# Kernel tuning notes

Hardware: AMD Instinct MI355X
Metric: run time of the kernel (lower is better)

## Reference

```python
import jax, jax.numpy as jnp
import numpy as np

OBS, ACT, HID, MIX, TOPK = 64, 16, 256, 16, 4
EPS = 1e-5

def _ln(x, g, b):
    m = jnp.mean(x, axis=-1, keepdims=True)
    v = jnp.mean(jnp.square(x - m), axis=-1, keepdims=True)
    return (x - m) * jax.lax.rsqrt(v + EPS) * g + b

def setup_inputs() -> dict:
    key = jax.random.key(0)
    ks = jax.random.split(key, 12)
    B = 16384
    D = OBS + ACT            # 80
    F = HID * MIX            # 4096
    s = lambda fan_in: 1.0 / np.sqrt(fan_in)
    return {
        "x": jax.random.normal(ks[0], (B, OBS), jnp.float32),
        "a": jax.random.normal(ks[1], (B, ACT), jnp.float32),
        "W1": jax.random.uniform(ks[2], (F, D), jnp.float32, -s(D), s(D)),
        "b1": jnp.zeros((F,), jnp.float32),
        "W2": jax.random.uniform(ks[3], (F, F), jnp.float32, -s(F), s(F)),
        "b2": jnp.zeros((F,), jnp.float32),
        "W3": jax.random.uniform(ks[4], (1, HID), jnp.float32, -s(HID), s(HID)),
        "b3": jnp.zeros((1,), jnp.float32),
        "g1": jnp.ones((F,), jnp.float32),
        "be1": jnp.zeros((F,), jnp.float32),
        "g2": jnp.ones((F,), jnp.float32),
        "be2": jnp.zeros((F,), jnp.float32),
        "Wg": jax.random.uniform(ks[5], (MIX, D), jnp.float32, -s(D), s(D)),
        "bg": jnp.zeros((MIX,), jnp.float32),
    }

def reference(x, a, W1, b1, W2, b2, W3, b3, g1, be1, g2, be2, Wg, bg):
    B = x.shape[0]
    xa = jnp.concatenate([x, a], axis=1)                      # [B, D]
    gate_scores = jax.nn.softmax(xa @ Wg.T + bg, axis=-1)     # [B, MIX]
    topk_vals, topk_idx = jax.lax.top_k(gate_scores, TOPK)    # [B, K]
    # renormalize top-k weights, scatter into dense score tensor
    topk_vals = topk_vals / jnp.sum(topk_vals, axis=-1, keepdims=True)
    scores = jnp.zeros_like(gate_scores).at[
        jnp.arange(B)[:, None], topk_idx].set(topk_vals)      # [B, MIX]
    h = jax.nn.relu(_ln(xa @ W1.T + b1, g1, be1))             # [B, HID*MIX]
    h = jax.nn.relu(_ln(h @ W2.T + b2, g2, be2))              # [B, HID*MIX]
    h = h.reshape(B, HID, MIX)                                # row-major, same as torch
    h = jnp.mean(h * scores[:, None, :], axis=-1)             # [B, HID]
    return h @ W3.T + b3                                      # [B, 1]
```

## Files before the change

### kernel.cpp

```cpp
#include <hip/hip_runtime.h>
#include <stdint.h>

#define OBS 64
#define ACTD 16
#define DIN 80
#define MIX 16
#define FF 4096
#define NB 16384
#define CHUNK 4096
#define KP 96
#define LNEPS 1e-5f

typedef float f32x4 __attribute__((ext_vector_type(4)));
typedef short bf16x8 __attribute__((ext_vector_type(8)));

__device__ __forceinline__ unsigned short f2bf(float f) {
    union { float f; uint32_t u; } v; v.f = f;
    uint32_t u = v.u;
    u += 0x7fff + ((u >> 16) & 1);
    return (unsigned short)(u >> 16);
}
__device__ __forceinline__ float bf2f(unsigned short h) {
    union { uint32_t u; float f; } v; v.u = ((uint32_t)h) << 16;
    return v.f;
}

__global__ __launch_bounds__(256) void k_conv(const float* __restrict__ W,
                                              unsigned short* __restrict__ O, int n4) {
    int i = blockIdx.x * 256 + threadIdx.x;
    if (i >= n4) return;
    float4 v = ((const float4*)W)[i];
    ushort4 o;
    o.x = f2bf(v.x); o.y = f2bf(v.y); o.z = f2bf(v.z); o.w = f2bf(v.w);
    ((ushort4*)O)[i] = o;
}

__global__ __launch_bounds__(256) void k_prep_x(const float* __restrict__ x, const float* __restrict__ a,
                                                unsigned short* __restrict__ xab) {
    int row = blockIdx.x * 256 + threadIdx.x;
    const float4* xp = (const float4*)(x + (size_t)row * OBS);
    unsigned short* o = xab + (size_t)row * KP;
#pragma unroll
    for (int i = 0; i < 16; ++i) {
        float4 v = xp[i];
        ushort4 u; u.x = f2bf(v.x); u.y = f2bf(v.y); u.z = f2bf(v.z); u.w = f2bf(v.w);
        ((ushort4*)o)[i] = u;
    }
    const float4* ap = (const float4*)(a + (size_t)row * ACTD);
#pragma unroll
    for (int i = 0; i < 4; ++i) {
        float4 v = ap[i];
        ushort4 u; u.x = f2bf(v.x); u.y = f2bf(v.y); u.z = f2bf(v.z); u.w = f2bf(v.w);
        ((ushort4*)(o + OBS))[i] = u;
    }
    ushort4 t0; t0.x = 0x3F80; t0.y = 0; t0.z = 0; t0.w = 0;
    ushort4 z;  z.x = 0; z.y = 0; z.z = 0; z.w = 0;
    ((ushort4*)(o + 80))[0] = t0;
    ((ushort4*)(o + 84))[0] = z;
    ((ushort4*)(o + 88))[0] = z;
    ((ushort4*)(o + 92))[0] = z;
}

__global__ __launch_bounds__(256) void k_prep_w1(const float* __restrict__ W1, const float* __restrict__ b1,
                                                 unsigned short* __restrict__ W1b) {
    int f = blockIdx.x * 256 + threadIdx.x;
    const float4* wp = (const float4*)(W1 + (size_t)f * DIN);
    unsigned short* o = W1b + (size_t)f * KP;
#pragma unroll
    for (int i = 0; i < 20; ++i) {
        float4 v = wp[i];
        ushort4 u; u.x = f2bf(v.x); u.y = f2bf(v.y); u.z = f2bf(v.z); u.w = f2bf(v.w);
        ((ushort4*)o)[i] = u;
    }
    ushort4 t0; t0.x = f2bf(b1[f]); t0.y = 0; t0.z = 0; t0.w = 0;
    ushort4 z;  z.x = 0; z.y = 0; z.z = 0; z.w = 0;
    ((ushort4*)(o + 80))[0] = t0;
    ((ushort4*)(o + 84))[0] = z;
    ((ushort4*)(o + 88))[0] = z;
    ((ushort4*)(o + 92))[0] = z;
}

__global__ __launch_bounds__(256) void k_gate(const float* __restrict__ x, const float* __restrict__ a,
                                              const float* __restrict__ Wg, const float* __restrict__ bg,
                                              float* __restrict__ scores) {
    __shared__ float wgs[MIX * DIN];
    __shared__ float bgs[MIX];
    int t = threadIdx.x;
    for (int e = t; e < MIX * DIN; e += 256) wgs[e] = Wg[e];
    if (t < MIX) bgs[t] = bg[t];
    __syncthreads();
    int row = blockIdx.x * 256 + t;
    float xa[DIN];
    const float4* xp = (const float4*)(x + (size_t)row * OBS);
#pragma unroll
    for (int i = 0; i < OBS / 4; ++i) {
        float4 v = xp[i];
        xa[i*4] = v.x; xa[i*4+1] = v.y; xa[i*4+2] = v.z; xa[i*4+3] = v.w;
    }
    const float4* ap = (const float4*)(a + (size_t)row * ACTD);
#pragma unroll
    for (int i = 0; i < ACTD / 4; ++i) {
        float4 v = ap[i];
        xa[OBS+i*4] = v.x; xa[OBS+i*4+1] = v.y; xa[OBS+i*4+2] = v.z; xa[OBS+i*4+3] = v.w;
    }
    double p[MIX];
    double mx = -1e300;
#pragma unroll
    for (int m = 0; m < MIX; ++m) {
        double acc = (double)bgs[m];
#pragma unroll
        for (int k = 0; k < DIN; ++k) acc += (double)xa[k] * (double)wgs[m*DIN + k];
        p[m] = acc;
        if (acc > mx) mx = acc;
    }
#pragma unroll
    for (int m = 0; m < MIX; ++m) p[m] = exp(p[m] - mx);
    unsigned used = 0;
    double s4 = 0.0;
#pragma unroll
    for (int j = 0; j < 4; ++j) {
        int best = 0; double bv = -1.0;
#pragma unroll
        for (int m = 0; m < MIX; ++m)
            if (!((used >> m) & 1) && p[m] > bv) { bv = p[m]; best = m; }
        used |= 1u << best;
        s4 += bv;
    }
    float* so = scores + (size_t)row * MIX;
#pragma unroll
    for (int m = 0; m < MIX; ++m)
        so[m] = ((used >> m) & 1) ? (float)(p[m] / s4) : 0.f;
}

__global__ __launch_bounds__(256) void k_gemm1(const unsigned short* __restrict__ A,
                                               const unsigned short* __restrict__ B,
                                               unsigned short* __restrict__ C,
                                               float* __restrict__ pstats) {
    __shared__ alignas(16) unsigned short As[128 * 32];
    __shared__ alignas(16) unsigned short Bs[128 * 32];
    int t = threadIdx.x;
    int pm = blockIdx.x & 31;
    int pn = blockIdx.x >> 5;
    int lane = t & 63, wid = t >> 6, wm = wid >> 1, wn = wid & 1;

    const unsigned short* Ap = A + (size_t)pm * 128 * KP;
    const unsigned short* Bp = B + (size_t)pn * 128 * KP;

    f32x4 acc[4][4] = {};

    for (int k0 = 0; k0 < KP; k0 += 32) {
#pragma unroll
        for (int i = 0; i < 2; ++i) {
            int u = t + i * 256;
            int row = u >> 2, p = u & 3;
            int ls = p ^ ((row >> 1) & 3);
            __builtin_amdgcn_global_load_lds(
                (const __attribute__((address_space(1))) void*)(Ap + (size_t)row * KP + k0 + ls * 8),
                (__attribute__((address_space(3))) void*)(As + u * 8), 16, 0, 0);
            __builtin_amdgcn_global_load_lds(
                (const __attribute__((address_space(1))) void*)(Bp + (size_t)row * KP + k0 + ls * 8),
                (__attribute__((address_space(3))) void*)(Bs + u * 8), 16, 0, 0);
        }
        __syncthreads();
        bf16x8 af[4], bfr[4];
#pragma unroll
        for (int mf = 0; mf < 4; ++mf) {
            int r = wm * 64 + mf * 16 + (lane & 15);
            int p = (lane >> 4) ^ ((r >> 1) & 3);
            af[mf] = *(const bf16x8*)(As + r * 32 + p * 8);
        }
#pragma unroll
        for (int nf = 0; nf < 4; ++nf) {
            int r = wn * 64 + nf * 16 + (lane & 15);
            int p = (lane >> 4) ^ ((r >> 1) & 3);
            bfr[nf] = *(const bf16x8*)(Bs + r * 32 + p * 8);
        }
#pragma unroll
        for (int mf = 0; mf < 4; ++mf)
#pragma unroll
            for (int nf = 0; nf < 4; ++nf)
                acc[mf][nf] = __builtin_amdgcn_mfma_f32_16x16x32_bf16(af[mf], bfr[nf], acc[mf][nf], 0, 0, 0);
        __syncthreads();
    }

    int rowbase = pm * 128 + wm * 64 + (lane >> 4) * 4;
    int colbase = pn * 128 + wn * 64 + (lane & 15);
#pragma unroll
    for (int mf = 0; mf < 4; ++mf) {
#pragma unroll
        for (int rr = 0; rr < 4; ++rr) {
            float ss = 0.f, qq = 0.f;
#pragma unroll
            for (int nf = 0; nf < 4; ++nf) {
                float v = acc[mf][nf][rr];
                ss += v; qq += v * v;
                C[(size_t)(rowbase + mf * 16 + rr) * FF + colbase + nf * 16] = f2bf(v);
            }
#pragma unroll
            for (int mask = 1; mask <= 8; mask <<= 1) {
                ss += __shfl_xor(ss, mask);
                qq += __shfl_xor(qq, mask);
            }
            if ((lane & 15) == 0) {
                int row = rowbase + mf * 16 + rr;
                int j = pn * 2 + wn;
                pstats[((size_t)row * 64 + j) * 2 + 0] = ss;
                pstats[((size_t)row * 64 + j) * 2 + 1] = qq;
            }
        }
    }
}

__global__ __launch_bounds__(256) void k_ln1(unsigned short* __restrict__ h1,
                                             const float* __restrict__ pstats,
                                             const float* __restrict__ g1, const float* __restrict__ be1) {
    __shared__ float st[8][2];
    int t = threadIdx.x;
    int r0 = blockIdx.x * 8;
    if (t < 8) {
        float s = 0.f, q = 0.f;
        const float* pp = pstats + (size_t)(r0 + t) * 128;
#pragma unroll
        for (int j = 0; j < 64; ++j) { s += pp[j * 2]; q += pp[j * 2 + 1]; }
        float mu = s / (float)FF;
        float var = q / (float)FF - mu * mu;
        st[t][0] = mu;
        st[t][1] = rsqrtf(var + LNEPS);
    }
    __syncthreads();
    int c = t * 16;
    float g[16], b[16];
#pragma unroll
    for (int q = 0; q < 4; ++q) {
        float4 gv = *(const float4*)(g1 + c + q * 4);
        float4 bv = *(const float4*)(be1 + c + q * 4);
        g[q*4] = gv.x; g[q*4+1] = gv.y; g[q*4+2] = gv.z; g[q*4+3] = gv.w;
        b[q*4] = bv.x; b[q*4+1] = bv.y; b[q*4+2] = bv.z; b[q*4+3] = bv.w;
    }
    for (int r = 0; r < 8; ++r) {
        float mu = st[r][0], rs = st[r][1];
        unsigned short* hp = h1 + (size_t)(r0 + r) * FF + c;
        uint4 u0 = *(const uint4*)hp;
        uint4 u1 = *(const uint4*)(hp + 8);
        uint32_t uu[8] = {u0.x, u0.y, u0.z, u0.w, u1.x, u1.y, u1.z, u1.w};
        uint32_t oo[8];
#pragma unroll
        for (int q = 0; q < 8; ++q) {
            float v0 = bf2f((unsigned short)(uu[q] & 0xffff));
            float v1 = bf2f((unsigned short)(uu[q] >> 16));
            float o0 = fmaxf((v0 - mu) * rs * g[q*2]   + b[q*2],   0.f);
            float o1 = fmaxf((v1 - mu) * rs * g[q*2+1] + b[q*2+1], 0.f);
            oo[q] = (uint32_t)f2bf(o0) | ((uint32_t)f2bf(o1) << 16);
        }
        uint4 w0; w0.x = oo[0]; w0.y = oo[1]; w0.z = oo[2]; w0.w = oo[3];
        uint4 w1; w1.x = oo[4]; w1.y = oo[5]; w1.z = oo[6]; w1.w = oo[7];
        *(uint4*)hp = w0;
        *(uint4*)(hp + 8) = w1;
    }
}

__global__ __launch_bounds__(512, 1) void k_gemm2(const unsigned short* __restrict__ A,
                                                  const unsigned short* __restrict__ B,
                                                  unsigned short* __restrict__ C) {
    constexpr int K = FF;
    constexpr int NKT = K / 64;
    __shared__ alignas(16) unsigned short As[2][2][8192];
    __shared__ alignas(16) unsigned short Bs[2][2][8192];

    int t = threadIdx.x;
    int lane = t & 63, wid = t >> 6;
    int wm = wid >> 2, wn = wid & 3;

    int bid = blockIdx.x;
    int xcd = bid & 7, w = bid >> 3;
    int pm = (xcd >> 1) * 4 + (w >> 3);
    int pn = (xcd & 1) * 8 + (w & 7);

    const unsigned short* Ap = A + (size_t)pm * 256 * K;
    const unsigned short* Bp = B + (size_t)pn * 256 * K;

    int l15 = lane & 15, l4 = lane >> 4;
    int slk0 = (l4 ^ (l15 & 7)) * 16;
    int slk1 = ((4 + l4) ^ (l15 & 7)) * 16;
    const char* Abase = (const char*)&As[0][0][0];
    const char* Bbase = (const char*)&Bs[0][0][0];
    const char* afp0 = Abase + wm * 16384 + l15 * 128 + slk0;
    const char* afp1 = Abase + wm * 16384 + l15 * 128 + slk1;
    const char* bfp0 = Bbase + (wn >> 1) * 16384 + (wn & 1) * 8192 + l15 * 128 + slk0;
    const char* bfp1 = Bbase + (wn >> 1) * 16384 + (wn & 1) * 8192 + l15 * 128 + slk1;

    int r0 = t >> 3;
    int swz = ((t & 7) ^ (r0 & 7)) * 8;
    const unsigned short* sA0 = Ap + (size_t)(r0)       * K + swz;
    const unsigned short* sA1 = Ap + (size_t)(64 + r0)  * K + swz;
    const unsigned short* sA2 = Ap + (size_t)(128 + r0) * K + swz;
    const unsigned short* sA3 = Ap + (size_t)(192 + r0) * K + swz;
    const unsigned short* sB0 = Bp + (size_t)(r0)       * K + swz;
    const unsigned short* sB1 = Bp + (size_t)(64 + r0)  * K + swz;
    const unsigned short* sB2 = Bp + (size_t)(128 + r0) * K + swz;
    const unsigned short* sB3 = Bp + (size_t)(192 + r0) * K + swz;
    char* dA = (char*)&As[0][0][0] + t * 16;
    char* dB = (char*)&Bs[0][0][0] + t * 16;

    f32x4 acc[8][4] = {};
    bf16x8 af[4][2], bfr[4][2];

#define STG_A(BUF, HH, p0, p1)                                                              \
    __builtin_amdgcn_global_load_lds((const __attribute__((address_space(1))) void*)(p0),   \
        (__attribute__((address_space(3))) void*)(dA + (BUF)*32768 + (HH)*16384), 16, 0, 0);\
    __builtin_amdgcn_global_load_lds((const __attribute__((address_space(1))) void*)(p1),   \
        (__attribute__((address_space(3))) void*)(dA + (BUF)*32768 + (HH)*16384 + 8192), 16, 0, 0);
#define STG_B(BUF, HH, p0, p1)                                                              \
    __builtin_amdgcn_global_load_lds((const __attribute__((address_space(1))) void*)(p0),   \
        (__attribute__((address_space(3))) void*)(dB + (BUF)*32768 + (HH)*16384), 16, 0, 0);\
    __builtin_amdgcn_global_load_lds((const __attribute__((address_space(1))) void*)(p1),   \
        (__attribute__((address_space(3))) void*)(dB + (BUF)*32768 + (HH)*16384 + 8192), 16, 0, 0);

#define RD_AF(BUF, MH)                                                                      \
    _Pragma("unroll") for (int m = 0; m < 4; ++m) {                                         \
        af[m][0] = *(const bf16x8*)(afp0 + (BUF)*32768 + (MH)*8192 + m*2048);               \
        af[m][1] = *(const bf16x8*)(afp1 + (BUF)*32768 + (MH)*8192 + m*2048);               \
    }
#define RD_BF(BUF)                                                                          \
    _Pragma("unroll") for (int n2 = 0; n2 < 4; ++n2) {                                      \
        bfr[n2][0] = *(const bf16x8*)(bfp0 + (BUF)*32768 + n2*2048);                        \
        bfr[n2][1] = *(const bf16x8*)(bfp1 + (BUF)*32768 + n2*2048);                        \
    }

#define MFMA_Q(MB, NLO)                                                                     \
    __builtin_amdgcn_s_setprio(1);                                                          \
    _Pragma("unroll") for (int kk = 0; kk < 2; ++kk)                                        \
    _Pragma("unroll") for (int m = 0; m < 4; ++m)                                           \
    _Pragma("unroll") for (int n = (NLO); n < (NLO) + 2; ++n)                               \
        acc[(MB)*4 + m][n] = __builtin_amdgcn_mfma_f32_16x16x32_bf16(                       \
            af[m][kk], bfr[n][kk], acc[(MB)*4 + m][n], 0, 0, 0);                            \
    __builtin_amdgcn_s_setprio(0);                                                          \
    __builtin_amdgcn_sched_barrier(0);

#define TILE(BUF, DO_STAGE)                                                                 \
    if (DO_STAGE) { STG_A(1 - (BUF), 0, sA0, sA1) }                                         \
    if (DO_STAGE) asm volatile("s_waitcnt vmcnt(2)" ::: "memory");                          \
    else          asm volatile("s_waitcnt vmcnt(0)" ::: "memory");                          \
    __builtin_amdgcn_s_barrier();                                                           \
    __builtin_amdgcn_sched_barrier(0);                                                      \
    RD_AF(BUF, 0) RD_BF(BUF)                                                                \
    MFMA_Q(0, 0)                                                                            \
    if (DO_STAGE) { STG_A(1 - (BUF), 1, sA2, sA3) }                                         \
    MFMA_Q(0, 2)                                                                            \
    if (DO_STAGE) { STG_B(1 - (BUF), 0, sB0, sB1) }                                         \
    RD_AF(BUF, 1)                                                                           \
    MFMA_Q(1, 0)                                                                            \
    if (DO_STAGE) { STG_B(1 - (BUF), 1, sB2, sB3) }                                         \
    MFMA_Q(1, 2)                                                                            \
    asm volatile("" ::: "memory");                                                          \
    __builtin_amdgcn_s_barrier();                                                           \
    asm volatile("" ::: "memory");                                                          \
    if (DO_STAGE) { sA0 += 64; sA1 += 64; sA2 += 64; sA3 += 64;                             \
                    sB0 += 64; sB1 += 64; sB2 += 64; sB3 += 64; }

    STG_A(0, 0, sA0, sA1) STG_A(0, 1, sA2, sA3)
    STG_B(0, 0, sB0, sB1) STG_B(0, 1, sB2, sB3)
    sA0 += 64; sA1 += 64; sA2 += 64; sA3 += 64;
    sB0 += 64; sB1 += 64; sB2 += 64; sB3 += 64;
    asm volatile("" ::: "memory");

    for (int i = 0; i < NKT / 2 - 1; ++i) {
        TILE(0, true)
        TILE(1, true)
    }
    TILE(0, true)
    TILE(1, false)

#undef STG_A
#undef STG_B
#undef RD_AF
#undef RD_BF
#undef MFMA_Q
#undef TILE

    int row0 = pm * 256 + wm * 128 + (lane >> 4) * 4;
    int col0 = pn * 256 + wn * 64 + (lane & 15);
#pragma unroll
    for (int gm = 0; gm < 8; ++gm)
#pragma unroll
        for (int gn = 0; gn < 4; ++gn)
#pragma unroll
            for (int rr = 0; rr < 4; ++rr)
                C[(size_t)(row0 + gm * 16 + rr) * FF + col0 + gn * 16] = f2bf(acc[gm][gn][rr]);
}

__global__ __launch_bounds__(256) void k_epi(const unsigned short* __restrict__ y2,
                                             const float* __restrict__ scores,
                                             const float* __restrict__ b2,
                                             const float* __restrict__ g2, const float* __restrict__ be2,
                                             const float* __restrict__ W3, const float* __restrict__ b3,
                                             float* __restrict__ out) {
    int row = blockIdx.x, t = threadIdx.x;
    int lane = t & 63, wid = t >> 6;
    __shared__ float sS[MIX];
    __shared__ float rA[4], rB[4];
    __shared__ float stats[2];
    const unsigned short* yp = y2 + (size_t)row * FF + t * 16;
    uint4 u0 = *(const uint4*)yp;
    uint4 u1 = *(const uint4*)(yp + 8);
    float v[16];
    v[0]  = bf2f((unsigned short)(u0.x & 0xffff)); v[1]  = bf2f((unsigned short)(u0.x >> 16));
    v[2]  = bf2f((unsigned short)(u0.y & 0xffff)); v[3]  = bf2f((unsigned short)(u0.y >> 16));
    v[4]  = bf2f((unsigned short)(u0.z & 0xffff)); v[5]  = bf2f((unsigned short)(u0.z >> 16));
    v[6]  = bf2f((unsigned short)(u0.w & 0xffff)); v[7]  = bf2f((unsigned short)(u0.w >> 16));
    v[8]  = bf2f((unsigned short)(u1.x & 0xffff)); v[9]  = bf2f((unsigned short)(u1.x >> 16));
    v[10] = bf2f((unsigned short)(u1.y & 0xffff)); v[11] = bf2f((unsigned short)(u1.y >> 16));
    v[12] = bf2f((unsigned short)(u1.z & 0xffff)); v[13] = bf2f((unsigned short)(u1.z >> 16));
    v[14] = bf2f((unsigned short)(u1.w & 0xffff)); v[15] = bf2f((unsigned short)(u1.w >> 16));
    const float* b2p = b2 + t * 16;
#pragma unroll
    for (int blk = 0; blk < 4; ++blk) {
        float4 q = *(const float4*)(b2p + blk * 4);
        v[blk*4+0] += q.x; v[blk*4+1] += q.y; v[blk*4+2] += q.z; v[blk*4+3] += q.w;
    }
    if (t < MIX) sS[t] = scores[(size_t)row * MIX + t];
    float s = 0.f, sq = 0.f;
#pragma unroll
    for (int j = 0; j < 16; ++j) { s += v[j]; sq += v[j] * v[j]; }
#pragma unroll
    for (int off = 32; off >= 1; off >>= 1) {
        s  += __shfl_down(s, off);
        sq += __shfl_down(sq, off);
    }
    if (lane == 0) { rA[wid] = s; rB[wid] = sq; }
    __syncthreads();
    if (t == 0) {
        float S = rA[0] + rA[1] + rA[2] + rA[3];
        float Q = rB[0] + rB[1] + rB[2] + rB[3];
        float mu = S / (float)FF;
        float var = Q / (float)FF - mu * mu;
        stats[0] = mu;
        stats[1] = rsqrtf(var + LNEPS);
    }
    __syncthreads();
    float mu = stats[0], rs = stats[1];
    const float* gp = g2 + t * 16;
    const float* bp = be2 + t * 16;
    float accum = 0.f;
#pragma unroll
    for (int blk = 0; blk < 4; ++blk) {
        float4 gg = *(const float4*)(gp + blk * 4);
        float4 bb = *(const float4*)(bp + blk * 4);
        float ga[4] = {gg.x, gg.y, gg.z, gg.w};
        float ba[4] = {bb.x, bb.y, bb.z, bb.w};
#pragma unroll
        for (int jj = 0; jj < 4; ++jj) {
            int m = blk * 4 + jj;
            float o = (v[m] - mu) * rs * ga[jj] + ba[jj];
            o = fmaxf(o, 0.f);
            accum += o * sS[m];
        }
    }
    float part = accum * W3[t] * 0.0625f;
#pragma unroll
    for (int off = 32; off >= 1; off >>= 1) part += __shfl_down(part, off);
    if (lane == 0) rA[wid] = part;
    __syncthreads();
    if (t == 0) out[row] = rA[0] + rA[1] + rA[2] + rA[3] + b3[0];
}

extern "C" void kernel_launch(void* const* d_in, const int* in_sizes, int n_in,
                              void* d_out, int out_size, void* d_ws, size_t ws_size,
                              hipStream_t stream) {
    const float* x   = (const float*)d_in[0];
    const float* a   = (const float*)d_in[1];
    const float* W1  = (const float*)d_in[2];
    const float* b1  = (const float*)d_in[3];
    const float* W2  = (const float*)d_in[4];
    const float* b2  = (const float*)d_in[5];
    const float* W3  = (const float*)d_in[6];
    const float* b3  = (const float*)d_in[7];
    const float* g1  = (const float*)d_in[8];
    const float* be1 = (const float*)d_in[9];
    const float* g2  = (const float*)d_in[10];
    const float* be2 = (const float*)d_in[11];
    const float* Wg  = (const float*)d_in[12];
    const float* bg  = (const float*)d_in[13];
    float* out = (float*)d_out;

    char* ws = (char*)d_ws;
    unsigned short* W2b    = (unsigned short*)ws;
    float*          scores = (float*)(ws + 33554432ull);
    unsigned short* h1c    = (unsigned short*)(ws + 34603008ull);
    unsigned short* y2c    = (unsigned short*)(ws + 68157440ull);
    unsigned short* xabc   = (unsigned short*)(ws + 68157440ull);
    unsigned short* W1b    = (unsigned short*)(ws + 68157440ull + 786432ull);
    float*          pstats = (float*)(ws + 68157440ull + 1572864ull);

    k_conv<<<(FF * FF / 4 + 255) / 256, 256, 0, stream>>>(W2, W2b, FF * FF / 4);
    k_gate<<<NB / 256, 256, 0, stream>>>(x, a, Wg, bg, scores);

    for (int c = 0; c < NB / CHUNK; ++c) {
        const float* xc = x + (size_t)c * CHUNK * OBS;
        const float* ac = a + (size_t)c * CHUNK * ACTD;
        const float* sc = scores + (size_t)c * CHUNK * MIX;
        float* oc = out + (size_t)c * CHUNK;
        k_prep_x<<<CHUNK / 256, 256, 0, stream>>>(xc, ac, xabc);
        k_prep_w1<<<FF / 256, 256, 0, stream>>>(W1, b1, W1b);
        k_gemm1<<<(CHUNK / 128) * (FF / 128), 256, 0, stream>>>(xabc, W1b, h1c, pstats);
        k_ln1<<<CHUNK / 8, 256, 0, stream>>>(h1c, pstats, g1, be1);
        k_gemm2<<<(CHUNK / 256) * (FF / 256), 512, 0, stream>>>(h1c, W2b, y2c);
        k_epi<<<CHUNK, 256, 0, stream>>>(y2c, sc, b2, g2, be2, W3, b3, oc);
    }
}
```

Before: 742.6 us.

## Restructure GEMM main loop into finer-grained LDS staging with per-quarter barriers

```diff
diff --git a/kernel.cpp b/kernel.cpp
--- a/kernel.cpp
+++ b/kernel.cpp
@@ -321,62 +321,79 @@
         af[m][0] = *(const bf16x8*)(afp0 + (BUF)*32768 + (MH)*8192 + m*2048);               \
         af[m][1] = *(const bf16x8*)(afp1 + (BUF)*32768 + (MH)*8192 + m*2048);               \
     }
-#define RD_BF(BUF)                                                                          \
-    _Pragma("unroll") for (int n2 = 0; n2 < 4; ++n2) {                                      \
-        bfr[n2][0] = *(const bf16x8*)(bfp0 + (BUF)*32768 + n2*2048);                        \
-        bfr[n2][1] = *(const bf16x8*)(bfp1 + (BUF)*32768 + n2*2048);                        \
-    }
-
-#define MFMA_Q(MB, NLO)                                                                     \
+#define RD_BF2(BUF, NP)                                                                     \
+    _Pragma("unroll") for (int n2 = 0; n2 < 2; ++n2) {                                      \
+        bfr[(NP)*2 + n2][0] = *(const bf16x8*)(bfp0 + (BUF)*32768 + ((NP)*2 + n2)*2048);    \
+        bfr[(NP)*2 + n2][1] = *(const bf16x8*)(bfp1 + (BUF)*32768 + ((NP)*2 + n2)*2048);    \
+    }
+
+#define MFMA_Q(MB, NP)                                                                      \
+    __builtin_amdgcn_s_barrier();                                                           \
+    asm volatile("s_waitcnt lgkmcnt(0)" ::: "memory");                                      \
+    __builtin_amdgcn_sched_barrier(0);                                                      \
     __builtin_amdgcn_s_setprio(1);                                                          \
     _Pragma("unroll") for (int kk = 0; kk < 2; ++kk)                                        \
     _Pragma("unroll") for (int m = 0; m < 4; ++m)                                           \
-    _Pragma("unroll") for (int n = (NLO); n < (NLO) + 2; ++n)                               \
-        acc[(MB)*4 + m][n] = __builtin_amdgcn_mfma_f32_16x16x32_bf16(                       \
-            af[m][kk], bfr[n][kk], acc[(MB)*4 + m][n], 0, 0, 0);                            \
+    _Pragma("unroll") for (int n = 0; n < 2; ++n)                                           \
+        acc[(MB)*4 + m][(NP)*2 + n] = __builtin_amdgcn_mfma_f32_16x16x32_bf16(              \
+            af[m][kk], bfr[(NP)*2 + n][kk], acc[(MB)*4 + m][(NP)*2 + n], 0, 0, 0);          \
     __builtin_amdgcn_s_setprio(0);                                                          \
     __builtin_amdgcn_sched_barrier(0);
-
-#define TILE(BUF, DO_STAGE)                                                                 \
-    if (DO_STAGE) { STG_A(1 - (BUF), 0, sA0, sA1) }                                         \
-    if (DO_STAGE) asm volatile("s_waitcnt vmcnt(2)" ::: "memory");                          \
-    else          asm volatile("s_waitcnt vmcnt(0)" ::: "memory");                          \
-    __builtin_amdgcn_s_barrier();                                                           \
-    __builtin_amdgcn_sched_barrier(0);                                                      \
-    RD_AF(BUF, 0) RD_BF(BUF)                                                                \
-    MFMA_Q(0, 0)                                                                            \
-    if (DO_STAGE) { STG_A(1 - (BUF), 1, sA2, sA3) }                                         \
-    MFMA_Q(0, 2)                                                                            \
-    if (DO_STAGE) { STG_B(1 - (BUF), 0, sB0, sB1) }                                         \
-    RD_AF(BUF, 1)                                                                           \
-    MFMA_Q(1, 0)                                                                            \
-    if (DO_STAGE) { STG_B(1 - (BUF), 1, sB2, sB3) }                                         \
-    MFMA_Q(1, 2)                                                                            \
-    asm volatile("" ::: "memory");                                                          \
-    __builtin_amdgcn_s_barrier();                                                           \
-    asm volatile("" ::: "memory");                                                          \
-    if (DO_STAGE) { sA0 += 64; sA1 += 64; sA2 += 64; sA3 += 64;                             \
-                    sB0 += 64; sB1 += 64; sB2 += 64; sB3 += 64; }
 
     STG_A(0, 0, sA0, sA1) STG_A(0, 1, sA2, sA3)
     STG_B(0, 0, sB0, sB1) STG_B(0, 1, sB2, sB3)
     sA0 += 64; sA1 += 64; sA2 += 64; sA3 += 64;
     sB0 += 64; sB1 += 64; sB2 += 64; sB3 += 64;
-    asm volatile("" ::: "memory");
-
-    for (int i = 0; i < NKT / 2 - 1; ++i) {
-        TILE(0, true)
-        TILE(1, true)
-    }
-    TILE(0, true)
-    TILE(1, false)
-
+    STG_B(1, 0, sB0, sB1) STG_B(1, 1, sB2, sB3)
+    sB0 += 64; sB1 += 64; sB2 += 64; sB3 += 64;
+    asm volatile("s_waitcnt vmcnt(4)" ::: "memory");
+    __builtin_amdgcn_s_barrier();
+
+    for (int i = 0; i < NKT / 2; ++i) {
+        RD_AF(0, 0) RD_BF2(0, 0)
+        STG_A(1, 0, sA0, sA1)
+        MFMA_Q(0, 0)
+        __builtin_amdgcn_s_barrier();
+        RD_BF2(0, 1)
+        STG_A(1, 1, sA2, sA3)
+        MFMA_Q(0, 1)
+        __builtin_amdgcn_s_barrier();
+        sA0 += 64; sA1 += 64; sA2 += 64; sA3 += 64;
+        RD_AF(0, 1)
+        STG_B(0, 0, sB0, sB1)
+        MFMA_Q(1, 0)
+        __builtin_amdgcn_s_barrier();
+        STG_B(0, 1, sB2, sB3)
+        MFMA_Q(1, 1)
+        asm volatile("s_waitcnt vmcnt(4)" ::: "memory");
+        __builtin_amdgcn_s_barrier();
+        sB0 += 64; sB1 += 64; sB2 += 64; sB3 += 64;
+
+        RD_AF(1, 0) RD_BF2(1, 0)
+        STG_A(0, 0, sA0, sA1)
+        MFMA_Q(0, 0)
+        __builtin_amdgcn_s_barrier();
+        RD_BF2(1, 1)
+        STG_A(0, 1, sA2, sA3)
+        MFMA_Q(0, 1)
+        __builtin_amdgcn_s_barrier();
+        sA0 += 64; sA1 += 64; sA2 += 64; sA3 += 64;
+        RD_AF(1, 1)
+        STG_B(1, 0, sB0, sB1)
+        MFMA_Q(1, 0)
+        __builtin_amdgcn_s_barrier();
+        STG_B(1, 1, sB2, sB3)
+        MFMA_Q(1, 1)
+        asm volatile("s_waitcnt vmcnt(4)" ::: "memory");
+        __builtin_amdgcn_s_barrier();
+        sB0 += 64; sB1 += 64; sB2 += 64; sB3 += 64;
+    }
+    asm volatile("s_waitcnt vmcnt(0)" ::: "memory");
 #undef STG_A
 #undef STG_B
 #undef RD_AF
-#undef RD_BF
+#undef RD_BF2
 #undef MFMA_Q
-#undef TILE
 
     int row0 = pm * 256 + wm * 128 + (lane >> 4) * 4;
     int col0 = pn * 256 + wn * 64 + (lane & 15);
```

New measurement: 758.1 us. 1.02x slower.
